# Optimization experiments

Measured on AMD Instinct MI355X. Metric: run time of the kernel, lower is better.

Reference implementation:

```python
import jax, jax.numpy as jnp
import numpy as np

B, S, I, H, A = 512, 256, 12, 256, 9


def _lstm_layer(x, w_ih, w_hh, b_ih, b_hh):
    # x: [B,S,in] -> outputs [B,S,H], final (h, c). PyTorch gate order i,f,g,o.
    b, s, _ = x.shape
    h_dim = w_hh.shape[1]
    xg = jnp.einsum('bsi,gi->bsg', x, w_ih) + b_ih  # [B,S,4H] precomputed input gates

    def step(carry, xg_t):
        h, c = carry
        gates = xg_t + h @ w_hh.T + b_hh
        i_g, f_g, g_g, o_g = jnp.split(gates, 4, axis=-1)
        c = jax.nn.sigmoid(f_g) * c + jax.nn.sigmoid(i_g) * jnp.tanh(g_g)
        h = jax.nn.sigmoid(o_g) * jnp.tanh(c)
        return (h, c), h

    init = (jnp.zeros((b, h_dim), x.dtype), jnp.zeros((b, h_dim), x.dtype))
    (h, c), ys = jax.lax.scan(step, init, jnp.swapaxes(xg, 0, 1))
    return jnp.swapaxes(ys, 0, 1), h, c


def setup_inputs() -> dict:
    key = jax.random.key(0)
    ks = jax.random.split(key, 20)
    sc = 0.1
    inp = {
        'x': jax.random.normal(ks[0], (B, S, I), jnp.float32),
        'mask': jnp.ones((B, A), jnp.float32),
        'W_emb': jax.random.normal(ks[1], (H, I), jnp.float32) * sc,
        'b_emb': jnp.zeros((H,), jnp.float32),
        'w_ih0': jax.random.normal(ks[2], (4 * H, H), jnp.float32) * sc,
        'w_hh0': jax.random.normal(ks[3], (4 * H, H), jnp.float32) * sc,
        'b_ih0': jnp.zeros((4 * H,), jnp.float32),
        'b_hh0': jnp.zeros((4 * H,), jnp.float32),
        'w_ih1': jax.random.normal(ks[4], (4 * H, H), jnp.float32) * sc,
        'w_hh1': jax.random.normal(ks[5], (4 * H, H), jnp.float32) * sc,
        'b_ih1': jnp.zeros((4 * H,), jnp.float32),
        'b_hh1': jnp.zeros((4 * H,), jnp.float32),
        'ln_g': jnp.ones((H,), jnp.float32),
        'ln_b': jnp.zeros((H,), jnp.float32),
        'w1': jax.random.normal(ks[6], (32, H), jnp.float32) * sc,
        'b1': jnp.zeros((32,), jnp.float32),
        'w2': jax.random.normal(ks[7], (A, 32), jnp.float32) * sc,
        'b2': jnp.zeros((A,), jnp.float32),
    }
    return inp


def reference(x, mask, W_emb, b_emb, w_ih0, w_hh0, b_ih0, b_hh0,
              w_ih1, w_hh1, b_ih1, b_hh1, ln_g, ln_b, w1, b1, w2, b2):
    # embed + ReLU
    emb = jax.nn.relu(jnp.einsum('bsi,hi->bsh', x, W_emb) + b_emb)  # [B,S,H]
    # 2-layer LSTM (dropout between layers is identity in eval mode)
    y0, h0, c0 = _lstm_layer(emb, w_ih0, w_hh0, b_ih0, b_hh0)
    y1, h1, c1 = _lstm_layer(y0, w_ih1, w_hh1, b_ih1, b_hh1)
    last = y1[:, -1, :]  # [B,H]
    # LayerNorm
    mu = jnp.mean(last, axis=-1, keepdims=True)
    var = jnp.mean((last - mu) ** 2, axis=-1, keepdims=True)
    normed = (last - mu) / jnp.sqrt(var + 1e-5) * ln_g + ln_b
    # MLP head (dropout identity in eval)
    hdn = jax.nn.relu(normed @ w1.T + b1)
    logits = hdn @ w2.T + b2  # [B,A]
    logits = logits + (1.0 - mask) * -1e9
    hidden = (jnp.stack([h0, h1]), jnp.stack([c0, c1]))
    return logits, hidden
```

## Files before the change

kernel.cpp:

```cpp
#include <hip/hip_runtime.h>
#include <cstdint>
#include <cstddef>

typedef __attribute__((ext_vector_type(8))) short short8;
typedef __attribute__((ext_vector_type(4))) float f32x4;

#define MFMA16(a, b, c) __builtin_amdgcn_mfma_f32_16x16x32_bf16((a), (b), (c), 0, 0, 0)

constexpr int kB = 512, kS = 256, kI = 12, kH = 256, kA = 9;
constexpr int kNS = 8;
constexpr int kNB = 32;
constexpr int kT  = 512;
constexpr int LDH = 264;
constexpr int LDG = 132;
constexpr int kBH = kB * kH;
constexpr int FLS = 512;

constexpr int OUT_H = kB * kA;
constexpr int OUT_C = OUT_H + 2 * kBH;

__device__ __forceinline__ short f2bf(float f) {
  uint32_t u = __float_as_uint(f);
  u += 0x7fffu + ((u >> 16) & 1u);
  return (short)(u >> 16);
}
__device__ __forceinline__ float fast_sigmoid(float v) {
  return __builtin_amdgcn_rcpf(1.f + __expf(-v));
}
__device__ __forceinline__ float fast_tanh(float v) {
  return 2.f * __builtin_amdgcn_rcpf(1.f + __expf(-2.f * v)) - 1.f;
}

__global__ __launch_bounds__(kT, 2) void lstm_scan_kernel(
    const float* __restrict__ x,
    const float* __restrict__ W_emb, const float* __restrict__ b_emb,
    const float* __restrict__ w_ih0, const float* __restrict__ w_hh0,
    const float* __restrict__ b_ih0, const float* __restrict__ b_hh0,
    const float* __restrict__ w_ih1, const float* __restrict__ w_hh1,
    const float* __restrict__ b_ih1, const float* __restrict__ b_hh1,
    unsigned short* __restrict__ h0ex, unsigned short* __restrict__ h1ex,
    int* __restrict__ flags,
    float* __restrict__ dout)
{
  const int tid   = threadIdx.x;
  const int btile = blockIdx.x & (kNB - 1);
  const int slice = blockIdx.x >> 5;
  const int b0    = btile * 16;
  const int lane  = tid & 63;
  const int wave  = tid >> 6;
  const int n16   = lane & 15;
  const int quad  = lane >> 4;

  __shared__ short embL[16 * LDH];
  __shared__ short hA[16 * LDH];
  __shared__ short hB[16 * LDH];
  __shared__ float gL0[16 * LDG];
  __shared__ float gL1[16 * LDG];

  for (int i = tid; i < 16 * LDH; i += kT) { hA[i] = 0; hB[i] = 0; }

  const float* Wm[4] = { w_ih0, w_hh0, w_ih1, w_hh1 };
  short8 wB[4][8];
  {
    const int gcol = (wave >> 1) * kH + slice * 32 + (wave & 1) * 16 + n16;
#pragma unroll
    for (int mat = 0; mat < 4; ++mat) {
      const float* wp = Wm[mat] + (size_t)gcol * kH;
#pragma unroll
      for (int kk = 0; kk < 8; ++kk) {
        const float* p = wp + kk * 32 + quad * 8;
        const float4 f0 = *(const float4*)p;
        const float4 f1 = *(const float4*)(p + 4);
        short8 v;
        v[0] = f2bf(f0.x); v[1] = f2bf(f0.y); v[2] = f2bf(f0.z); v[3] = f2bf(f0.w);
        v[4] = f2bf(f1.x); v[5] = f2bf(f1.y); v[6] = f2bf(f1.z); v[7] = f2bf(f1.w);
        wB[mat][kk] = v;
      }
    }
  }
  short8 wE[2];
  float bembv[2];
#pragma unroll
  for (int i = 0; i < 2; ++i) {
    const int col = wave * 32 + i * 16 + n16;
    short8 v;
#pragma unroll
    for (int j = 0; j < 8; ++j) {
      const int k = quad * 8 + j;
      v[j] = (k < kI) ? f2bf(W_emb[col * kI + k]) : (short)0;
    }
    wE[i] = v;
    bembv[i] = b_emb[col];
  }
  const int erow = tid >> 5;
  const int ec   = tid & 31;
  const int ecol = slice * 32 + ec;
  float bi0[4], bi1[4];
#pragma unroll
  for (int g = 0; g < 4; ++g) {
    bi0[g] = b_ih0[g * kH + ecol] + b_hh0[g * kH + ecol];
    bi1[g] = b_ih1[g * kH + ecol] + b_hh1[g * kH + ecol];
  }
  float c0v = 0.f, c1v = 0.f;

  {
    const float* xr = x + (size_t)(b0 + n16) * kS * kI;
    short8 xa;
#pragma unroll
    for (int j = 0; j < 8; ++j) {
      const int k = quad * 8 + j;
      xa[j] = (k < kI) ? f2bf(xr[k]) : (short)0;
    }
#pragma unroll
    for (int i = 0; i < 2; ++i) {
      f32x4 z = {0.f, 0.f, 0.f, 0.f};
      f32x4 e = MFMA16(xa, wE[i], z);
      const int col = wave * 32 + i * 16 + n16;
#pragma unroll
      for (int r = 0; r < 4; ++r) {
        float v = e[r] + bembv[i];
        v = v > 0.f ? v : 0.f;
        embL[(quad * 4 + r) * LDH + col] = f2bf(v);
      }
    }
  }
  __syncthreads();

  int* const fl = flags + btile * FLS;

  for (int p = 0; p <= kS; ++p) {
    const int par = p & 1;

    {
      f32x4 a0 = {0.f,0.f,0.f,0.f}, g1 = a0;
#pragma unroll
      for (int kk = 0; kk < 8; ++kk) {
        const short8 ha = *(const short8*)&hA[n16 * LDH + kk * 32 + quad * 8];
        a0 = MFMA16(ha, wB[1][kk], a0);
        g1 = MFMA16(ha, wB[2][kk], g1);
      }
#pragma unroll
      for (int kk = 0; kk < 8; ++kk) {
        const short8 e = *(const short8*)&embL[n16 * LDH + kk * 32 + quad * 8];
        a0 = MFMA16(e, wB[0][kk], a0);
      }
#pragma unroll
      for (int kk = 0; kk < 8; ++kk) {
        const short8 hb = *(const short8*)&hB[n16 * LDH + kk * 32 + quad * 8];
        g1 = MFMA16(hb, wB[3][kk], g1);
      }
      const int lcol = (wave >> 1) * 32 + (wave & 1) * 16 + n16;
#pragma unroll
      for (int r = 0; r < 4; ++r) {
        gL0[(quad * 4 + r) * LDG + lcol] = a0[r];
        gL1[(quad * 4 + r) * LDG + lcol] = g1[r];
      }
    }
    __syncthreads();

    if (p < kS) {
      const float iv = gL0[erow * LDG +       ec] + bi0[0];
      const float fv = gL0[erow * LDG +  32 + ec] + bi0[1];
      const float gv = gL0[erow * LDG +  64 + ec] + bi0[2];
      const float ov = gL0[erow * LDG +  96 + ec] + bi0[3];
      const float c = fast_sigmoid(fv) * c0v + fast_sigmoid(iv) * fast_tanh(gv);
      c0v = c;
      const float h = fast_sigmoid(ov) * fast_tanh(c);
      unsigned short* dst = &h0ex[(size_t)par * kBH + (size_t)(b0 + erow) * kH + ecol];
      __hip_atomic_store(dst, (unsigned short)f2bf(h), __ATOMIC_RELAXED, __HIP_MEMORY_SCOPE_AGENT);
      if (p == kS - 1) {
        dout[OUT_H + (size_t)(b0 + erow) * kH + ecol] = h;
        dout[OUT_C + (size_t)(b0 + erow) * kH + ecol] = c;
      }
    }
    if (p >= 1) {
      const float iv = gL1[erow * LDG +       ec] + bi1[0];
      const float fv = gL1[erow * LDG +  32 + ec] + bi1[1];
      const float gv = gL1[erow * LDG +  64 + ec] + bi1[2];
      const float ov = gL1[erow * LDG +  96 + ec] + bi1[3];
      const float c = fast_sigmoid(fv) * c1v + fast_sigmoid(iv) * fast_tanh(gv);
      c1v = c;
      const float h = fast_sigmoid(ov) * fast_tanh(c);
      unsigned short* dst = &h1ex[(size_t)par * kBH + (size_t)(b0 + erow) * kH + ecol];
      __hip_atomic_store(dst, (unsigned short)f2bf(h), __ATOMIC_RELAXED, __HIP_MEMORY_SCOPE_AGENT);
      if (p == kS) {
        dout[OUT_H + kBH + (size_t)(b0 + erow) * kH + ecol] = h;
        dout[OUT_C + kBH + (size_t)(b0 + erow) * kH + ecol] = c;
      }
    }
    __syncthreads();

    if (p < kS) {
      if (tid == 0)
        __hip_atomic_fetch_add(fl + p, 1, __ATOMIC_RELAXED, __HIP_MEMORY_SCOPE_AGENT);

      if (p + 1 < kS) {
        const float* xr = x + ((size_t)(b0 + n16) * kS + (p + 1)) * kI;
        short8 xa;
#pragma unroll
        for (int j = 0; j < 8; ++j) {
          const int k = quad * 8 + j;
          xa[j] = (k < kI) ? f2bf(xr[k]) : (short)0;
        }
#pragma unroll
        for (int i = 0; i < 2; ++i) {
          f32x4 z = {0.f, 0.f, 0.f, 0.f};
          f32x4 e = MFMA16(xa, wE[i], z);
          const int col = wave * 32 + i * 16 + n16;
#pragma unroll
          for (int r = 0; r < 4; ++r) {
            float v = e[r] + bembv[i];
            v = v > 0.f ? v : 0.f;
            embL[(quad * 4 + r) * LDH + col] = f2bf(v);
          }
        }
      }

      while (__hip_atomic_load(fl + p, __ATOMIC_RELAXED, __HIP_MEMORY_SCOPE_AGENT) < kNS)
        __builtin_amdgcn_s_sleep(1);

      {
        const int rr = tid >> 5;
        const int cc = (tid & 31) * 8;
        const size_t base = (size_t)par * kBH + (size_t)(b0 + rr) * kH + cc;
        const uint64_t* s0 = (const uint64_t*)&h0ex[base];
        const uint64_t* s1 = (const uint64_t*)&h1ex[base];
        uint64_t va0 = __hip_atomic_load(s0 + 0, __ATOMIC_RELAXED, __HIP_MEMORY_SCOPE_AGENT);
        uint64_t va1 = __hip_atomic_load(s0 + 1, __ATOMIC_RELAXED, __HIP_MEMORY_SCOPE_AGENT);
        uint64_t vb0 = __hip_atomic_load(s1 + 0, __ATOMIC_RELAXED, __HIP_MEMORY_SCOPE_AGENT);
        uint64_t vb1 = __hip_atomic_load(s1 + 1, __ATOMIC_RELAXED, __HIP_MEMORY_SCOPE_AGENT);
        uint64_t* dA = (uint64_t*)&hA[rr * LDH + cc];
        uint64_t* dB = (uint64_t*)&hB[rr * LDH + cc];
        dA[0] = va0; dA[1] = va1;
        dB[0] = vb0; dB[1] = vb1;
      }
      __syncthreads();
    }
  }
}

__global__ __launch_bounds__(64) void head_kernel(
    const float* __restrict__ h1last, const float* __restrict__ mask,
    const float* __restrict__ ln_g, const float* __restrict__ ln_b,
    const float* __restrict__ w1, const float* __restrict__ b1,
    const float* __restrict__ w2, const float* __restrict__ b2,
    float* __restrict__ out)
{
  const int r = blockIdx.x;
  const int lane = threadIdx.x;
  __shared__ float ns[kH];
  __shared__ float hd[32];
  const float4 v = *(const float4*)&h1last[r * kH + lane * 4];
  float vv[4] = {v.x, v.y, v.z, v.w};
  float s = vv[0] + vv[1] + vv[2] + vv[3];
#pragma unroll
  for (int off = 32; off > 0; off >>= 1) s += __shfl_xor(s, off, 64);
  const float mean = s * (1.f / kH);
  float q = 0.f;
#pragma unroll
  for (int j = 0; j < 4; ++j) { const float d = vv[j] - mean; q += d * d; }
#pragma unroll
  for (int off = 32; off > 0; off >>= 1) q += __shfl_xor(q, off, 64);
  const float rstd = rsqrtf(q * (1.f / kH) + 1e-5f);
#pragma unroll
  for (int j = 0; j < 4; ++j) {
    const int c = lane * 4 + j;
    ns[c] = (vv[j] - mean) * rstd * ln_g[c] + ln_b[c];
  }
  __syncthreads();
  if (lane < 32) {
    float a = b1[lane];
    const float* wr = w1 + lane * kH;
    for (int k = 0; k < kH; ++k) a += ns[k] * wr[k];
    hd[lane] = a > 0.f ? a : 0.f;
  }
  __syncthreads();
  if (lane < kA) {
    float a = b2[lane];
    const float* wr = w2 + lane * 32;
#pragma unroll
    for (int k = 0; k < 32; ++k) a += hd[k] * wr[k];
    a += (1.f - mask[r * kA + lane]) * (-1e9f);
    out[r * kA + lane] = a;
  }
}

extern "C" void kernel_launch(void* const* d_in, const int* in_sizes, int n_in,
                              void* d_out, int out_size, void* d_ws, size_t ws_size,
                              hipStream_t stream)
{
  (void)in_sizes; (void)n_in; (void)out_size; (void)ws_size;
  const float* x     = (const float*)d_in[0];
  const float* mask  = (const float*)d_in[1];
  const float* W_emb = (const float*)d_in[2];
  const float* b_emb = (const float*)d_in[3];
  const float* w_ih0 = (const float*)d_in[4];
  const float* w_hh0 = (const float*)d_in[5];
  const float* b_ih0 = (const float*)d_in[6];
  const float* b_hh0 = (const float*)d_in[7];
  const float* w_ih1 = (const float*)d_in[8];
  const float* w_hh1 = (const float*)d_in[9];
  const float* b_ih1 = (const float*)d_in[10];
  const float* b_hh1 = (const float*)d_in[11];
  const float* ln_g  = (const float*)d_in[12];
  const float* ln_b  = (const float*)d_in[13];
  const float* w1    = (const float*)d_in[14];
  const float* b1    = (const float*)d_in[15];
  const float* w2    = (const float*)d_in[16];
  const float* b2    = (const float*)d_in[17];
  float* out = (float*)d_out;

  unsigned short* h0ex = (unsigned short*)d_ws;
  unsigned short* h1ex = h0ex + 2 * kBH;
  int* flags = (int*)(h1ex + 2 * kBH);
  const size_t flag_bytes = (size_t)kNB * FLS * sizeof(int);

  hipMemsetAsync(flags, 0, flag_bytes, stream);
  hipMemsetAsync(h1ex, 0, (size_t)kBH * sizeof(unsigned short), stream);

  lstm_scan_kernel<<<dim3(kNB * kNS), dim3(kT), 0, stream>>>(
      x, W_emb, b_emb, w_ih0, w_hh0, b_ih0, b_hh0, w_ih1, w_hh1, b_ih1, b_hh1,
      h0ex, h1ex, flags, out);

  head_kernel<<<dim3(kB), dim3(64), 0, stream>>>(
      out + OUT_H + kBH, mask, ln_g, ln_b, w1, b1, w2, b2, out);
}
```

Baseline: 1.012 ms.

## Replace flag-counter barrier with step-tagged hidden-state words polled directly

Each exchanged bf16 hidden value now travels in a 32-bit word with an 8-bit step tag, so consumers spin on the data itself rather than on a per-tile atomic counter. This removes one __syncthreads per step, the fetch_add and flag polling round trip, and the flag and buffer memsets. In exchange, exchange traffic doubles. Because the tags wrap modulo 256 and the workspace is never cleared, stale words from an earlier launch can match an expected tag, which risks early reads at the first steps.

New measurement: 1.056 ms. +4.4%, slower.

```diff
diff --git a/kernel.cpp b/kernel.cpp
--- a/kernel.cpp
+++ b/kernel.cpp
@@ -6,6 +6,8 @@
 typedef __attribute__((ext_vector_type(4))) float f32x4;
 
 #define MFMA16(a, b, c) __builtin_amdgcn_mfma_f32_16x16x32_bf16((a), (b), (c), 0, 0, 0)
+#define ALOAD64(p)   __hip_atomic_load((p), __ATOMIC_RELAXED, __HIP_MEMORY_SCOPE_AGENT)
+#define ASTORE32(p, v) __hip_atomic_store((p), (v), __ATOMIC_RELAXED, __HIP_MEMORY_SCOPE_AGENT)
 
 constexpr int kB = 512, kS = 256, kI = 12, kH = 256, kA = 9;
 constexpr int kNS = 8;
@@ -14,7 +16,6 @@
 constexpr int LDH = 264;
 constexpr int LDG = 132;
 constexpr int kBH = kB * kH;
-constexpr int FLS = 512;
 
 constexpr int OUT_H = kB * kA;
 constexpr int OUT_C = OUT_H + 2 * kBH;
@@ -38,8 +39,7 @@
     const float* __restrict__ b_ih0, const float* __restrict__ b_hh0,
     const float* __restrict__ w_ih1, const float* __restrict__ w_hh1,
     const float* __restrict__ b_ih1, const float* __restrict__ b_hh1,
-    unsigned short* __restrict__ h0ex, unsigned short* __restrict__ h1ex,
-    int* __restrict__ flags,
+    uint32_t* __restrict__ h0ex, uint32_t* __restrict__ h1ex,
     float* __restrict__ dout)
 {
   const int tid   = threadIdx.x;
@@ -126,10 +126,9 @@
   }
   __syncthreads();
 
-  int* const fl = flags + btile * FLS;
-
   for (int p = 0; p <= kS; ++p) {
     const int par = p & 1;
+    const uint32_t tag = (uint32_t)((p + 1) & 255);
 
     {
       f32x4 a0 = {0.f,0.f,0.f,0.f}, g1 = a0;
@@ -166,34 +165,33 @@
       const float c = fast_sigmoid(fv) * c0v + fast_sigmoid(iv) * fast_tanh(gv);
       c0v = c;
       const float h = fast_sigmoid(ov) * fast_tanh(c);
-      unsigned short* dst = &h0ex[(size_t)par * kBH + (size_t)(b0 + erow) * kH + ecol];
-      __hip_atomic_store(dst, (unsigned short)f2bf(h), __ATOMIC_RELAXED, __HIP_MEMORY_SCOPE_AGENT);
+      const uint32_t pk = ((uint32_t)(uint16_t)f2bf(h) << 16) | tag;
+      ASTORE32(&h0ex[(size_t)par * kBH + (size_t)(b0 + erow) * kH + ecol], pk);
       if (p == kS - 1) {
         dout[OUT_H + (size_t)(b0 + erow) * kH + ecol] = h;
         dout[OUT_C + (size_t)(b0 + erow) * kH + ecol] = c;
       }
     }
-    if (p >= 1) {
-      const float iv = gL1[erow * LDG +       ec] + bi1[0];
-      const float fv = gL1[erow * LDG +  32 + ec] + bi1[1];
-      const float gv = gL1[erow * LDG +  64 + ec] + bi1[2];
-      const float ov = gL1[erow * LDG +  96 + ec] + bi1[3];
-      const float c = fast_sigmoid(fv) * c1v + fast_sigmoid(iv) * fast_tanh(gv);
-      c1v = c;
-      const float h = fast_sigmoid(ov) * fast_tanh(c);
-      unsigned short* dst = &h1ex[(size_t)par * kBH + (size_t)(b0 + erow) * kH + ecol];
-      __hip_atomic_store(dst, (unsigned short)f2bf(h), __ATOMIC_RELAXED, __HIP_MEMORY_SCOPE_AGENT);
+    {
+      float h = 0.f;
+      if (p >= 1) {
+        const float iv = gL1[erow * LDG +       ec] + bi1[0];
+        const float fv = gL1[erow * LDG +  32 + ec] + bi1[1];
+        const float gv = gL1[erow * LDG +  64 + ec] + bi1[2];
+        const float ov = gL1[erow * LDG +  96 + ec] + bi1[3];
+        const float c = fast_sigmoid(fv) * c1v + fast_sigmoid(iv) * fast_tanh(gv);
+        c1v = c;
+        h = fast_sigmoid(ov) * fast_tanh(c);
+      }
+      const uint32_t pk = ((uint32_t)(uint16_t)f2bf(h) << 16) | tag;
+      ASTORE32(&h1ex[(size_t)par * kBH + (size_t)(b0 + erow) * kH + ecol], pk);
       if (p == kS) {
         dout[OUT_H + kBH + (size_t)(b0 + erow) * kH + ecol] = h;
-        dout[OUT_C + kBH + (size_t)(b0 + erow) * kH + ecol] = c;
-      }
-    }
-    __syncthreads();
+        dout[OUT_C + kBH + (size_t)(b0 + erow) * kH + ecol] = c1v;
+      }
+    }
 
     if (p < kS) {
-      if (tid == 0)
-        __hip_atomic_fetch_add(fl + p, 1, __ATOMIC_RELAXED, __HIP_MEMORY_SCOPE_AGENT);
-
       if (p + 1 < kS) {
         const float* xr = x + ((size_t)(b0 + n16) * kS + (p + 1)) * kI;
         short8 xa;
@@ -216,23 +214,35 @@
         }
       }
 
-      while (__hip_atomic_load(fl + p, __ATOMIC_RELAXED, __HIP_MEMORY_SCOPE_AGENT) < kNS)
-        __builtin_amdgcn_s_sleep(1);
-
       {
         const int rr = tid >> 5;
-        const int cc = (tid & 31) * 8;
-        const size_t base = (size_t)par * kBH + (size_t)(b0 + rr) * kH + cc;
+        const int cu = tid & 31;
+        const size_t base = (size_t)par * kBH + (size_t)(b0 + rr) * kH;
         const uint64_t* s0 = (const uint64_t*)&h0ex[base];
         const uint64_t* s1 = (const uint64_t*)&h1ex[base];
-        uint64_t va0 = __hip_atomic_load(s0 + 0, __ATOMIC_RELAXED, __HIP_MEMORY_SCOPE_AGENT);
-        uint64_t va1 = __hip_atomic_load(s0 + 1, __ATOMIC_RELAXED, __HIP_MEMORY_SCOPE_AGENT);
-        uint64_t vb0 = __hip_atomic_load(s1 + 0, __ATOMIC_RELAXED, __HIP_MEMORY_SCOPE_AGENT);
-        uint64_t vb1 = __hip_atomic_load(s1 + 1, __ATOMIC_RELAXED, __HIP_MEMORY_SCOPE_AGENT);
-        uint64_t* dA = (uint64_t*)&hA[rr * LDH + cc];
-        uint64_t* dB = (uint64_t*)&hB[rr * LDH + cc];
-        dA[0] = va0; dA[1] = va1;
-        dB[0] = vb0; dB[1] = vb1;
+        uint64_t v0[4], v1[4];
+        for (;;) {
+          bool ok = true;
+#pragma unroll
+          for (int k = 0; k < 4; ++k) v0[k] = ALOAD64(s0 + cu + 32 * k);
+#pragma unroll
+          for (int k = 0; k < 4; ++k) v1[k] = ALOAD64(s1 + cu + 32 * k);
+#pragma unroll
+          for (int k = 0; k < 4; ++k) {
+            ok = ok & (((uint32_t)v0[k] & 255u) == tag) & (((uint32_t)(v0[k] >> 32) & 255u) == tag);
+            ok = ok & (((uint32_t)v1[k] & 255u) == tag) & (((uint32_t)(v1[k] >> 32) & 255u) == tag);
+          }
+          if (ok) break;
+          __builtin_amdgcn_s_sleep(1);
+        }
+#pragma unroll
+        for (int k = 0; k < 4; ++k) {
+          const int c2 = cu * 2 + 64 * k;
+          hA[rr * LDH + c2]     = (short)((uint32_t)v0[k] >> 16);
+          hA[rr * LDH + c2 + 1] = (short)(v0[k] >> 48);
+          hB[rr * LDH + c2]     = (short)((uint32_t)v1[k] >> 16);
+          hB[rr * LDH + c2 + 1] = (short)(v1[k] >> 48);
+        }
       }
       __syncthreads();
     }
@@ -310,17 +320,12 @@
   const float* b2    = (const float*)d_in[17];
   float* out = (float*)d_out;
 
-  unsigned short* h0ex = (unsigned short*)d_ws;
-  unsigned short* h1ex = h0ex + 2 * kBH;
-  int* flags = (int*)(h1ex + 2 * kBH);
-  const size_t flag_bytes = (size_t)kNB * FLS * sizeof(int);
-
-  hipMemsetAsync(flags, 0, flag_bytes, stream);
-  hipMemsetAsync(h1ex, 0, (size_t)kBH * sizeof(unsigned short), stream);
+  uint32_t* h0ex = (uint32_t*)d_ws;
+  uint32_t* h1ex = h0ex + 2 * kBH;
 
   lstm_scan_kernel<<<dim3(kNB * kNS), dim3(kT), 0, stream>>>(
       x, W_emb, b_emb, w_ih0, w_hh0, b_ih0, b_hh0, w_ih1, w_hh1, b_ih1, b_hh1,
-      h0ex, h1ex, flags, out);
+      h0ex, h1ex, out);
 
   head_kernel<<<dim3(kB), dim3(64), 0, stream>>>(
       out + OUT_H + kBH, mask, ln_g, ln_b, w1, b1, w2, b2, out);
```

## Remap gate columns per wave and replace block barriers with per-wave flag publishes

Applied to the files above, without the earlier changes.

Each wave's MFMA columns now hold all four gates for four hidden units, so the gate math is done from a small per-wave scratch instead of a block-wide gate buffer behind two __syncthreads. The shared buffers for embedding and h state are double-buffered. Each wave publishes its own per-layer flag counter (64 arrivals instead of 8), so layer 0 can signal before layer 1 finishes. The goal is to cut intra-block barriers on the serial critical path, at the cost of more flag atomics and more fragile explicit waitcnt ordering.

After: 1.237 ms. 22.2% more time.

```diff
diff --git a/kernel.cpp b/kernel.cpp
--- a/kernel.cpp
+++ b/kernel.cpp
@@ -6,15 +6,19 @@
 typedef __attribute__((ext_vector_type(4))) float f32x4;
 
 #define MFMA16(a, b, c) __builtin_amdgcn_mfma_f32_16x16x32_bf16((a), (b), (c), 0, 0, 0)
+#define ALOADI(p)   __hip_atomic_load((p), __ATOMIC_RELAXED, __HIP_MEMORY_SCOPE_AGENT)
+#define ALOADU64(p) __hip_atomic_load((p), __ATOMIC_RELAXED, __HIP_MEMORY_SCOPE_AGENT)
+#define ASTOREU16(p, v) __hip_atomic_store((p), (v), __ATOMIC_RELAXED, __HIP_MEMORY_SCOPE_AGENT)
 
 constexpr int kB = 512, kS = 256, kI = 12, kH = 256, kA = 9;
 constexpr int kNS = 8;
 constexpr int kNB = 32;
 constexpr int kT  = 512;
 constexpr int LDH = 264;
-constexpr int LDG = 132;
+constexpr int LDT = 17;
 constexpr int kBH = kB * kH;
 constexpr int FLS = 512;
+constexpr int kPubs = kNS * 8;
 
 constexpr int OUT_H = kB * kA;
 constexpr int OUT_C = OUT_H + 2 * kBH;
@@ -51,18 +55,17 @@
   const int n16   = lane & 15;
   const int quad  = lane >> 4;
 
-  __shared__ short embL[16 * LDH];
-  __shared__ short hA[16 * LDH];
-  __shared__ short hB[16 * LDH];
-  __shared__ float gL0[16 * LDG];
-  __shared__ float gL1[16 * LDG];
-
-  for (int i = tid; i < 16 * LDH; i += kT) { hA[i] = 0; hB[i] = 0; }
+  __shared__ short emb2[2][16 * LDH];
+  __shared__ short hA2[2][16 * LDH];
+  __shared__ short hB2[2][16 * LDH];
+  __shared__ float scr[8 * 16 * LDT];
+
+  for (int i = tid; i < 16 * LDH; i += kT) { hA2[0][i] = 0; hB2[0][i] = 0; }
 
   const float* Wm[4] = { w_ih0, w_hh0, w_ih1, w_hh1 };
   short8 wB[4][8];
   {
-    const int gcol = (wave >> 1) * kH + slice * 32 + (wave & 1) * 16 + n16;
+    const int gcol = (n16 >> 2) * kH + slice * 32 + wave * 4 + (n16 & 3);
 #pragma unroll
     for (int mat = 0; mat < 4; ++mat) {
       const float* wp = Wm[mat] + (size_t)gcol * kH;
@@ -92,16 +95,18 @@
     wE[i] = v;
     bembv[i] = b_emb[col];
   }
-  const int erow = tid >> 5;
-  const int ec   = tid & 31;
-  const int ecol = slice * 32 + ec;
+  const int row_ew = quad * 4 + (n16 >> 2);
+  const int j_ew   = n16 & 3;
+  const int ucol   = slice * 32 + wave * 4 + j_ew;
+  const int grow   = b0 + row_ew;
   float bi0[4], bi1[4];
 #pragma unroll
   for (int g = 0; g < 4; ++g) {
-    bi0[g] = b_ih0[g * kH + ecol] + b_hh0[g * kH + ecol];
-    bi1[g] = b_ih1[g * kH + ecol] + b_hh1[g * kH + ecol];
+    bi0[g] = b_ih0[g * kH + ucol] + b_hh0[g * kH + ucol];
+    bi1[g] = b_ih1[g * kH + ucol] + b_hh1[g * kH + ucol];
   }
   float c0v = 0.f, c1v = 0.f;
+  float* const sw = scr + wave * (16 * LDT);
 
   {
     const float* xr = x + (size_t)(b0 + n16) * kS * kI;
@@ -120,117 +125,131 @@
       for (int r = 0; r < 4; ++r) {
         float v = e[r] + bembv[i];
         v = v > 0.f ? v : 0.f;
-        embL[(quad * 4 + r) * LDH + col] = f2bf(v);
+        emb2[0][(quad * 4 + r) * LDH + col] = f2bf(v);
       }
     }
   }
   __syncthreads();
 
-  int* const fl = flags + btile * FLS;
+  int* const f0 = flags + btile * FLS;
+  int* const f1 = f0 + 256;
 
   for (int p = 0; p <= kS; ++p) {
-    const int par = p & 1;
-
-    {
-      f32x4 a0 = {0.f,0.f,0.f,0.f}, g1 = a0;
-#pragma unroll
-      for (int kk = 0; kk < 8; ++kk) {
-        const short8 ha = *(const short8*)&hA[n16 * LDH + kk * 32 + quad * 8];
-        a0 = MFMA16(ha, wB[1][kk], a0);
-        g1 = MFMA16(ha, wB[2][kk], g1);
-      }
+    const int rpar  = p & 1;
+    const int wpar  = rpar ^ 1;
+    const int h1par = (p + 1) & 1;
+    const short* embL = emb2[rpar];
+    const short* hA   = hA2[rpar];
+    const short* hB   = hB2[rpar];
+
+    short8 haf[8];
+#pragma unroll
+    for (int kk = 0; kk < 8; ++kk)
+      haf[kk] = *(const short8*)&hA[n16 * LDH + kk * 32 + quad * 8];
+
+    if (p < kS) {
+      f32x4 a0 = {0.f, 0.f, 0.f, 0.f};
 #pragma unroll
       for (int kk = 0; kk < 8; ++kk) {
         const short8 e = *(const short8*)&embL[n16 * LDH + kk * 32 + quad * 8];
         a0 = MFMA16(e, wB[0][kk], a0);
       }
 #pragma unroll
-      for (int kk = 0; kk < 8; ++kk) {
-        const short8 hb = *(const short8*)&hB[n16 * LDH + kk * 32 + quad * 8];
-        g1 = MFMA16(hb, wB[3][kk], g1);
-      }
-      const int lcol = (wave >> 1) * 32 + (wave & 1) * 16 + n16;
-#pragma unroll
-      for (int r = 0; r < 4; ++r) {
-        gL0[(quad * 4 + r) * LDG + lcol] = a0[r];
-        gL1[(quad * 4 + r) * LDG + lcol] = g1[r];
-      }
-    }
-    __syncthreads();
-
-    if (p < kS) {
-      const float iv = gL0[erow * LDG +       ec] + bi0[0];
-      const float fv = gL0[erow * LDG +  32 + ec] + bi0[1];
-      const float gv = gL0[erow * LDG +  64 + ec] + bi0[2];
-      const float ov = gL0[erow * LDG +  96 + ec] + bi0[3];
+      for (int kk = 0; kk < 8; ++kk) a0 = MFMA16(haf[kk], wB[1][kk], a0);
+#pragma unroll
+      for (int r = 0; r < 4; ++r) sw[(quad * 4 + r) * LDT + n16] = a0[r];
+      const float iv = sw[row_ew * LDT +      j_ew] + bi0[0];
+      const float fv = sw[row_ew * LDT +  4 + j_ew] + bi0[1];
+      const float gv = sw[row_ew * LDT +  8 + j_ew] + bi0[2];
+      const float ov = sw[row_ew * LDT + 12 + j_ew] + bi0[3];
       const float c = fast_sigmoid(fv) * c0v + fast_sigmoid(iv) * fast_tanh(gv);
       c0v = c;
       const float h = fast_sigmoid(ov) * fast_tanh(c);
-      unsigned short* dst = &h0ex[(size_t)par * kBH + (size_t)(b0 + erow) * kH + ecol];
-      __hip_atomic_store(dst, (unsigned short)f2bf(h), __ATOMIC_RELAXED, __HIP_MEMORY_SCOPE_AGENT);
+      ASTOREU16(&h0ex[(size_t)rpar * kBH + (size_t)grow * kH + ucol],
+                (unsigned short)f2bf(h));
       if (p == kS - 1) {
-        dout[OUT_H + (size_t)(b0 + erow) * kH + ecol] = h;
-        dout[OUT_C + (size_t)(b0 + erow) * kH + ecol] = c;
-      }
-    }
+        dout[OUT_H + (size_t)grow * kH + ucol] = h;
+        dout[OUT_C + (size_t)grow * kH + ucol] = c;
+      }
+      __builtin_amdgcn_sched_barrier(0);
+      __builtin_amdgcn_s_waitcnt(0x0F70);
+      __builtin_amdgcn_sched_barrier(0);
+      if (lane == 0)
+        __hip_atomic_fetch_add(f0 + p, 1, __ATOMIC_RELAXED, __HIP_MEMORY_SCOPE_AGENT);
+    }
+
     if (p >= 1) {
-      const float iv = gL1[erow * LDG +       ec] + bi1[0];
-      const float fv = gL1[erow * LDG +  32 + ec] + bi1[1];
-      const float gv = gL1[erow * LDG +  64 + ec] + bi1[2];
-      const float ov = gL1[erow * LDG +  96 + ec] + bi1[3];
+      f32x4 a1 = {0.f, 0.f, 0.f, 0.f};
+#pragma unroll
+      for (int kk = 0; kk < 8; ++kk) a1 = MFMA16(haf[kk], wB[2][kk], a1);
+#pragma unroll
+      for (int kk = 0; kk < 8; ++kk) {
+        const short8 hb = *(const short8*)&hB[n16 * LDH + kk * 32 + quad * 8];
+        a1 = MFMA16(hb, wB[3][kk], a1);
+      }
+#pragma unroll
+      for (int r = 0; r < 4; ++r) sw[(quad * 4 + r) * LDT + n16] = a1[r];
+      const float iv = sw[row_ew * LDT +      j_ew] + bi1[0];
+      const float fv = sw[row_ew * LDT +  4 + j_ew] + bi1[1];
+      const float gv = sw[row_ew * LDT +  8 + j_ew] + bi1[2];
+      const float ov = sw[row_ew * LDT + 12 + j_ew] + bi1[3];
       const float c = fast_sigmoid(fv) * c1v + fast_sigmoid(iv) * fast_tanh(gv);
       c1v = c;
       const float h = fast_sigmoid(ov) * fast_tanh(c);
-      unsigned short* dst = &h1ex[(size_t)par * kBH + (size_t)(b0 + erow) * kH + ecol];
-      __hip_atomic_store(dst, (unsigned short)f2bf(h), __ATOMIC_RELAXED, __HIP_MEMORY_SCOPE_AGENT);
-      if (p == kS) {
-        dout[OUT_H + kBH + (size_t)(b0 + erow) * kH + ecol] = h;
-        dout[OUT_C + kBH + (size_t)(b0 + erow) * kH + ecol] = c;
-      }
-    }
-    __syncthreads();
-
+      if (p < kS) {
+        ASTOREU16(&h1ex[(size_t)h1par * kBH + (size_t)grow * kH + ucol],
+                  (unsigned short)f2bf(h));
+      } else {
+        dout[OUT_H + kBH + (size_t)grow * kH + ucol] = h;
+        dout[OUT_C + kBH + (size_t)grow * kH + ucol] = c;
+      }
+    } else {
+      ASTOREU16(&h1ex[(size_t)h1par * kBH + (size_t)grow * kH + ucol], (unsigned short)0);
+    }
     if (p < kS) {
-      if (tid == 0)
-        __hip_atomic_fetch_add(fl + p, 1, __ATOMIC_RELAXED, __HIP_MEMORY_SCOPE_AGENT);
-
-      if (p + 1 < kS) {
-        const float* xr = x + ((size_t)(b0 + n16) * kS + (p + 1)) * kI;
-        short8 xa;
-#pragma unroll
-        for (int j = 0; j < 8; ++j) {
-          const int k = quad * 8 + j;
-          xa[j] = (k < kI) ? f2bf(xr[k]) : (short)0;
+      __builtin_amdgcn_sched_barrier(0);
+      __builtin_amdgcn_s_waitcnt(0x0F70);
+      __builtin_amdgcn_sched_barrier(0);
+      if (lane == 0)
+        __hip_atomic_fetch_add(f1 + p, 1, __ATOMIC_RELAXED, __HIP_MEMORY_SCOPE_AGENT);
+    }
+
+    if (p + 1 < kS) {
+      const float* xr = x + ((size_t)(b0 + n16) * kS + (p + 1)) * kI;
+      short8 xa;
+#pragma unroll
+      for (int j = 0; j < 8; ++j) {
+        const int k = quad * 8 + j;
+        xa[j] = (k < kI) ? f2bf(xr[k]) : (short)0;
+      }
+#pragma unroll
+      for (int i = 0; i < 2; ++i) {
+        f32x4 z = {0.f, 0.f, 0.f, 0.f};
+        f32x4 e = MFMA16(xa, wE[i], z);
+        const int col = wave * 32 + i * 16 + n16;
+#pragma unroll
+        for (int r = 0; r < 4; ++r) {
+          float v = e[r] + bembv[i];
+          v = v > 0.f ? v : 0.f;
+          emb2[wpar][(quad * 4 + r) * LDH + col] = f2bf(v);
         }
-#pragma unroll
-        for (int i = 0; i < 2; ++i) {
-          f32x4 z = {0.f, 0.f, 0.f, 0.f};
-          f32x4 e = MFMA16(xa, wE[i], z);
-          const int col = wave * 32 + i * 16 + n16;
-#pragma unroll
-          for (int r = 0; r < 4; ++r) {
-            float v = e[r] + bembv[i];
-            v = v > 0.f ? v : 0.f;
-            embL[(quad * 4 + r) * LDH + col] = f2bf(v);
-          }
-        }
-      }
-
-      while (__hip_atomic_load(fl + p, __ATOMIC_RELAXED, __HIP_MEMORY_SCOPE_AGENT) < kNS)
-        __builtin_amdgcn_s_sleep(1);
-
+      }
+    }
+
+    if (p < kS) {
+      while (ALOADI(f0 + p) < kPubs) __builtin_amdgcn_s_sleep(1);
+      while (ALOADI(f1 + p) < kPubs) __builtin_amdgcn_s_sleep(1);
       {
         const int rr = tid >> 5;
         const int cc = (tid & 31) * 8;
-        const size_t base = (size_t)par * kBH + (size_t)(b0 + rr) * kH + cc;
-        const uint64_t* s0 = (const uint64_t*)&h0ex[base];
-        const uint64_t* s1 = (const uint64_t*)&h1ex[base];
-        uint64_t va0 = __hip_atomic_load(s0 + 0, __ATOMIC_RELAXED, __HIP_MEMORY_SCOPE_AGENT);
-        uint64_t va1 = __hip_atomic_load(s0 + 1, __ATOMIC_RELAXED, __HIP_MEMORY_SCOPE_AGENT);
-        uint64_t vb0 = __hip_atomic_load(s1 + 0, __ATOMIC_RELAXED, __HIP_MEMORY_SCOPE_AGENT);
-        uint64_t vb1 = __hip_atomic_load(s1 + 1, __ATOMIC_RELAXED, __HIP_MEMORY_SCOPE_AGENT);
-        uint64_t* dA = (uint64_t*)&hA[rr * LDH + cc];
-        uint64_t* dB = (uint64_t*)&hB[rr * LDH + cc];
+        const uint64_t* s0 = (const uint64_t*)&h0ex[(size_t)rpar * kBH + (size_t)(b0 + rr) * kH + cc];
+        const uint64_t* s1 = (const uint64_t*)&h1ex[(size_t)h1par * kBH + (size_t)(b0 + rr) * kH + cc];
+        uint64_t va0 = ALOADU64(s0 + 0);
+        uint64_t va1 = ALOADU64(s0 + 1);
+        uint64_t vb0 = ALOADU64(s1 + 0);
+        uint64_t vb1 = ALOADU64(s1 + 1);
+        uint64_t* dA = (uint64_t*)&hA2[wpar][rr * LDH + cc];
+        uint64_t* dB = (uint64_t*)&hB2[wpar][rr * LDH + cc];
         dA[0] = va0; dA[1] = va1;
         dB[0] = vb0; dB[1] = vb1;
       }
@@ -316,7 +335,6 @@
   const size_t flag_bytes = (size_t)kNB * FLS * sizeof(int);
 
   hipMemsetAsync(flags, 0, flag_bytes, stream);
-  hipMemsetAsync(h1ex, 0, (size_t)kBH * sizeof(unsigned short), stream);
 
   lstm_scan_kernel<<<dim3(kNB * kNS), dim3(kT), 0, stream>>>(
       x, W_emb, b_emb, w_ih0, w_hh0, b_ih0, b_hh0, w_ih1, w_hh1, b_ih1, b_hh1,
```
